# Optimization experiments

Measured on AMD Instinct MI355X. Metric: run time of the kernel, lower is better.

The kernel has to match this reference:

```python
import jax, jax.numpy as jnp
import numpy as np

STRIDE = (1, 1)
PAD = 1


def setup_inputs() -> dict:
    key = jax.random.key(0)
    k1, k2, k3 = jax.random.split(key, 3)
    X = jax.random.normal(k1, (32, 128, 56, 56), dtype=jnp.float32)
    weight = jax.random.normal(k2, (256, 128, 3, 3), dtype=jnp.float32) * 0.05
    bias = jax.random.normal(k3, (256,), dtype=jnp.float32) * 0.05
    return {"X": X, "weight": weight, "bias": bias}


def reference(X, weight, bias):
    # Equivalent to the naive 8-loop conv: standard 2D cross-correlation,
    # NCHW input, OIHW weight, stride 1, padding 1.
    out = jax.lax.conv_general_dilated(
        X, weight,
        window_strides=STRIDE,
        padding=[(PAD, PAD), (PAD, PAD)],
        dimension_numbers=("NCHW", "OIHW", "NCHW"),
    )
    out = out + bias[None, :, None, None]
    return out
```

## Files before the change

kernel.cpp:

```cpp
#include <hip/hip_runtime.h>
#include <hip/hip_bf16.h>


typedef __attribute__((ext_vector_type(8))) _Float16 half8;
typedef __attribute__((ext_vector_type(4))) float floatx4;

#define NN    32
#define CC    128
#define HH    56
#define WW    56
#define KOUT  256
#define HWs   3136
#define HP    58
#define HPP   (HP * HP)
#define XP_SHORTS ((size_t)NN * HPP * CC)
#define WT_SHORTS (36 * 8192)
#define WS_NEED ((XP_SHORTS + WT_SHORTS) * sizeof(short))

__device__ __forceinline__ void gload_lds16(const void* g, void* l) {
    __builtin_amdgcn_global_load_lds(
        (const __attribute__((address_space(1))) unsigned int*)g,
        (__attribute__((address_space(3))) unsigned int*)l, 16, 0, 0);
}

__global__ __launch_bounds__(256) void prep_x2(const float* __restrict__ X,
                                               short* __restrict__ Xp) {
    const int n   = blockIdx.x / HP;
    const int hp  = blockIdx.x % HP;
    const int tid = threadIdx.x;
    short* dst = Xp + ((size_t)n * HPP + (size_t)hp * HP) * CC;

    half8 z = {(_Float16)0.f, (_Float16)0.f, (_Float16)0.f, (_Float16)0.f,
               (_Float16)0.f, (_Float16)0.f, (_Float16)0.f, (_Float16)0.f};

    if (hp == 0 || hp == HP - 1) {
#pragma unroll
        for (int it = 0; it < 4; ++it) {
            const int u = it * 256 + tid;
            if (u < 928) *(half8*)&dst[u * 8] = z;
        }
        return;
    }

    const int h = hp - 1;
    __shared__ float xl[128 * 57];
    const float* src = X + (size_t)n * CC * HWs + h * WW;
#pragma unroll
    for (int i = 0; i < 7; ++i) {
        const int idx = i * 256 + tid;
        const int c   = idx / 14;
        const int w4  = idx - c * 14;
        const floatx4 v = *(const floatx4*)&src[(size_t)c * HWs + w4 * 4];
#pragma unroll
        for (int k = 0; k < 4; ++k) xl[c * 57 + w4 * 4 + k] = v[k];
    }
    __syncthreads();
#pragma unroll
    for (int it = 0; it < 4; ++it) {
        const int u = it * 256 + tid;
        if (u < 896) {
            const int oct = u & 15, w = u >> 4;
            _Float16 v[8];
#pragma unroll
            for (int j = 0; j < 8; ++j)
                v[j] = (_Float16)xl[(oct * 8 + j) * 57 + w];
            *(half8*)&dst[(w + 1) * CC + oct * 8] = *(half8*)v;
        } else if (u < 928) {
            const int q = u - 896;
            const int oct = q & 15;
            const int wpad = (q >> 4) ? (HP - 1) : 0;
            *(half8*)&dst[wpad * CC + oct * 8] = z;
        }
    }
}

__global__ __launch_bounds__(256) void prep_w3(const float* __restrict__ Wsrc,
                                               short* __restrict__ Wt) {
    const int gid = blockIdx.x * 256 + threadIdx.x;
    const int t2  = gid >> 10;
    const int u8  = gid & 1023;
    const int r   = u8 >> 3;
    const int o   = u8 & 7;
    const int rs  = t2 >> 2;
    const int ct  = (t2 >> 1) & 1;
    const int kb  = t2 & 1;
    const int k   = kb * 128 + r;
    const int c0  = ct * 64 + ((o ^ (r & 7)) << 3);
    _Float16 v[8];
#pragma unroll
    for (int j = 0; j < 8; ++j)
        v[j] = (_Float16)Wsrc[((size_t)k * CC + c0 + j) * 9 + rs];
    *(half8*)&Wt[(size_t)t2 * 8192 + u8 * 8] = *(half8*)v;
}

__global__ __launch_bounds__(256, 3) void conv_mfma4(
    const short* __restrict__ Xp, const short* __restrict__ Wt,
    const float* __restrict__ bias, float* __restrict__ out) {

    __shared__ __align__(16) short smem[16384];

    const int tid  = threadIdx.x;
    const int lane = tid & 63;
    const int wid  = tid >> 6;
    const int wr   = wid >> 1;
    const int wc   = wid & 1;
    const int bid  = blockIdx.x;
    const int kblk = blockIdx.y;
    const int pblk = (bid & 7) * 98 + (bid >> 3);

    const int swzoct = (lane & 7) ^ (lane >> 3);
    const short* vsrc[4];
#pragma unroll
    for (int i = 0; i < 4; ++i) {
        const int row = wid * 32 + i * 8 + (lane >> 3);
        const int p   = pblk * 128 + row;
        const int n   = p / HWs;
        const int hw  = p % HWs;
        const int h   = hw / WW;
        const int w   = hw % WW;
        vsrc[i] = Xp + ((size_t)n * HPP + (h + 1) * HP + (w + 1)) * CC + swzoct * 8;
    }

    floatx4 acc[4][4];
#pragma unroll
    for (int i = 0; i < 4; i++)
#pragma unroll
        for (int j = 0; j < 4; j++) acc[i][j] = (floatx4)(0.0f);

    for (int k = 0; k < 18; ++k) {
        const int rs = k >> 1, ct = k & 1;
        const int tap = ((rs / 3 - 1) * HP + (rs % 3 - 1)) * CC + ct * 64;

        if (k) __syncthreads();

        const short* as_ = Wt + (size_t)(k * 2 + kblk) * 8192 + wid * 2048 + lane * 8;
#pragma unroll
        for (int i = 0; i < 4; ++i)
            gload_lds16(as_ + i * 512, &smem[wid * 2048 + i * 512]);
#pragma unroll
        for (int i = 0; i < 4; ++i)
            gload_lds16(vsrc[i] + tap, &smem[8192 + wid * 2048 + i * 512]);

        __syncthreads();

#pragma unroll
        for (int ksub = 0; ksub < 2; ++ksub) {
            const int koct = ksub * 4 + (lane >> 4);
            half8 ah[4], bh[4];
#pragma unroll
            for (int mt = 0; mt < 4; ++mt) {
                const int ar = wr * 64 + mt * 16 + (lane & 15);
                ah[mt] = *(const half8*)&smem[ar * 64 + ((koct ^ (ar & 7)) << 3)];
            }
#pragma unroll
            for (int nt = 0; nt < 4; ++nt) {
                const int br = wc * 64 + nt * 16 + (lane & 15);
                bh[nt] = *(const half8*)&smem[8192 + br * 64 + ((koct ^ (br & 7)) << 3)];
            }
#pragma unroll
            for (int mt = 0; mt < 4; ++mt)
#pragma unroll
                for (int nt = 0; nt < 4; ++nt)
                    acc[mt][nt] = __builtin_amdgcn_mfma_f32_16x16x32_f16(
                        ah[mt], bh[nt], acc[mt][nt], 0, 0, 0);
        }
    }

#pragma unroll
    for (int mt = 0; mt < 4; ++mt) {
        const int ch = kblk * 128 + wr * 64 + mt * 16 + ((lane >> 4) << 2);
#pragma unroll
        for (int nt = 0; nt < 4; ++nt) {
            const int p  = pblk * 128 + wc * 64 + nt * 16 + (lane & 15);
            const int n  = p / HWs;
            const int hw = p % HWs;
            float* ob = out + ((size_t)n * KOUT + ch) * HWs + hw;
#pragma unroll
            for (int r = 0; r < 4; ++r)
                ob[(size_t)r * HWs] = acc[mt][nt][r] + bias[ch + r];
        }
    }
}

__global__ __launch_bounds__(256) void conv_naive(const float* __restrict__ X,
                                                  const float* __restrict__ Wt,
                                                  const float* __restrict__ bias,
                                                  float* __restrict__ out) {
    long o = (long)blockIdx.x * 256 + threadIdx.x;
    int w_ = o % WW;
    long t1 = o / WW;
    int h_ = t1 % HH;
    long t2 = t1 / HH;
    int k_ = t2 % KOUT;
    int n_ = (int)(t2 / KOUT);
    float acc = bias[k_];
    for (int c = 0; c < CC; ++c)
        for (int r = 0; r < 3; ++r) {
            int ih = h_ + r - 1;
            if ((unsigned)ih >= 56u) continue;
            for (int s = 0; s < 3; ++s) {
                int iw = w_ + s - 1;
                if ((unsigned)iw >= 56u) continue;
                acc += X[((long)(n_ * CC + c) * HH + ih) * WW + iw] *
                       Wt[((k_ * CC + c) * 3 + r) * 3 + s];
            }
        }
    out[o] = acc;
}

extern "C" void kernel_launch(void* const* d_in, const int* in_sizes, int n_in,
                              void* d_out, int out_size, void* d_ws, size_t ws_size,
                              hipStream_t stream) {
    const float* X    = (const float*)d_in[0];
    const float* Wsrc = (const float*)d_in[1];
    const float* bias = (const float*)d_in[2];
    float* out        = (float*)d_out;

    if (ws_size >= WS_NEED) {
        short* Xp = (short*)d_ws;
        short* Wt = Xp + XP_SHORTS;
        prep_x2<<<NN * HP, 256, 0, stream>>>(X, Xp);
        prep_w3<<<144, 256, 0, stream>>>(Wsrc, Wt);
        conv_mfma4<<<dim3(784, 2), 256, 0, stream>>>(Xp, Wt, bias, out);
    } else {
        conv_naive<<<100352, 256, 0, stream>>>(X, Wsrc, bias, out);
    }
}
```

Before: 213.3 us.

## Triple-buffer LDS pipeline with 512-thread 256-channel tiles and fused prep kernel

The conv kernel now computes all 256 output channels per block with 8 waves, so the grid no longer splits output channels and each input tile is loaded once. A three-stage LDS ring buffer with split half-loads, vmcnt waits and barriers overlaps global-to-LDS copies with MFMA work. MFMA sections are wrapped in s_setprio. The two prep kernels are merged into one launch, and the weight layout is changed to match. Costs are larger dynamic LDS (144KB), fewer blocks per CU, and a per-call hipFuncSetAttribute on the host.

```diff
diff --git a/kernel.cpp b/kernel.cpp
--- a/kernel.cpp
+++ b/kernel.cpp
@@ -14,8 +14,10 @@
 #define HP    58
 #define HPP   (HP * HP)
 #define XP_SHORTS ((size_t)NN * HPP * CC)
-#define WT_SHORTS (36 * 8192)
+#define WT_SHORTS (18 * 16384)
 #define WS_NEED ((XP_SHORTS + WT_SHORTS) * sizeof(short))
+#define BUF_HALFS 24576
+#define LDS_BYTES (3 * BUF_HALFS * 2)
 
 __device__ __forceinline__ void gload_lds16(const void* g, void* l) {
     __builtin_amdgcn_global_load_lds(
@@ -23,11 +25,33 @@
         (__attribute__((address_space(3))) unsigned int*)l, 16, 0, 0);
 }
 
-__global__ __launch_bounds__(256) void prep_x2(const float* __restrict__ X,
-                                               short* __restrict__ Xp) {
-    const int n   = blockIdx.x / HP;
-    const int hp  = blockIdx.x % HP;
+__global__ __launch_bounds__(256) void prep_fused(const float* __restrict__ X,
+                                                  const float* __restrict__ Wsrc,
+                                                  short* __restrict__ Xp,
+                                                  short* __restrict__ Wt) {
+    __shared__ float xl[128 * 57];
     const int tid = threadIdx.x;
+
+    if (blockIdx.x < 144) {
+        const int gid  = blockIdx.x * 256 + tid;
+        const int tile = gid >> 11;
+        const int u    = gid & 2047;
+        const int r    = u >> 3;
+        const int o    = u & 7;
+        const int tap  = tile >> 1;
+        const int ct   = tile & 1;
+        const int c0   = ct * 64 + ((o ^ (r & 7)) << 3);
+        _Float16 v[8];
+#pragma unroll
+        for (int j = 0; j < 8; ++j)
+            v[j] = (_Float16)Wsrc[((size_t)r * CC + c0 + j) * 9 + tap];
+        *(half8*)&Wt[(size_t)tile * 16384 + u * 8] = *(half8*)v;
+        return;
+    }
+
+    const int xb = blockIdx.x - 144;
+    const int n  = xb / HP;
+    const int hp = xb % HP;
     short* dst = Xp + ((size_t)n * HPP + (size_t)hp * HP) * CC;
 
     half8 z = {(_Float16)0.f, (_Float16)0.f, (_Float16)0.f, (_Float16)0.f,
@@ -43,7 +67,6 @@
     }
 
     const int h = hp - 1;
-    __shared__ float xl[128 * 57];
     const float* src = X + (size_t)n * CC * HWs + h * WW;
 #pragma unroll
     for (int i = 0; i < 7; ++i) {
@@ -74,30 +97,11 @@
     }
 }
 
-__global__ __launch_bounds__(256) void prep_w3(const float* __restrict__ Wsrc,
-                                               short* __restrict__ Wt) {
-    const int gid = blockIdx.x * 256 + threadIdx.x;
-    const int t2  = gid >> 10;
-    const int u8  = gid & 1023;
-    const int r   = u8 >> 3;
-    const int o   = u8 & 7;
-    const int rs  = t2 >> 2;
-    const int ct  = (t2 >> 1) & 1;
-    const int kb  = t2 & 1;
-    const int k   = kb * 128 + r;
-    const int c0  = ct * 64 + ((o ^ (r & 7)) << 3);
-    _Float16 v[8];
-#pragma unroll
-    for (int j = 0; j < 8; ++j)
-        v[j] = (_Float16)Wsrc[((size_t)k * CC + c0 + j) * 9 + rs];
-    *(half8*)&Wt[(size_t)t2 * 8192 + u8 * 8] = *(half8*)v;
-}
-
-__global__ __launch_bounds__(256, 3) void conv_mfma4(
+__global__ __launch_bounds__(512, 2) void conv_mfma5(
     const short* __restrict__ Xp, const short* __restrict__ Wt,
     const float* __restrict__ bias, float* __restrict__ out) {
 
-    __shared__ __align__(16) short smem[16384];
+    extern __shared__ __align__(16) short smem[];
 
     const int tid  = threadIdx.x;
     const int lane = tid & 63;
@@ -105,14 +109,13 @@
     const int wr   = wid >> 1;
     const int wc   = wid & 1;
     const int bid  = blockIdx.x;
-    const int kblk = blockIdx.y;
     const int pblk = (bid & 7) * 98 + (bid >> 3);
 
     const int swzoct = (lane & 7) ^ (lane >> 3);
-    const short* vsrc[4];
-#pragma unroll
-    for (int i = 0; i < 4; ++i) {
-        const int row = wid * 32 + i * 8 + (lane >> 3);
+    const short* vsrc[2];
+#pragma unroll
+    for (int i = 0; i < 2; ++i) {
+        const int row = wid * 16 + i * 8 + (lane >> 3);
         const int p   = pblk * 128 + row;
         const int n   = p / HWs;
         const int hw  = p % HWs;
@@ -121,54 +124,105 @@
         vsrc[i] = Xp + ((size_t)n * HPP + (h + 1) * HP + (w + 1)) * CC + swzoct * 8;
     }
 
+    const int aoff = wid * 2048 + lane * 8;
+
+#define STAGE_P0(kk, bb) do {                                                  \
+    const short* as_ = Wt + (size_t)(kk) * 16384 + aoff;                       \
+    gload_lds16(as_,        &smem[(bb) + aoff]);                               \
+    gload_lds16(as_ + 512,  &smem[(bb) + aoff + 512]);                         \
+    const int rs_ = (kk) >> 1;                                                 \
+    const int tap_ = ((rs_ / 3 - 1) * HP + (rs_ % 3 - 1)) * CC + ((kk) & 1) * 64; \
+    gload_lds16(vsrc[0] + tap_, &smem[(bb) + 16384 + wid * 1024 + lane * 8]);  \
+} while (0)
+#define STAGE_P1(kk, bb) do {                                                  \
+    const short* as_ = Wt + (size_t)(kk) * 16384 + aoff;                       \
+    gload_lds16(as_ + 1024, &smem[(bb) + aoff + 1024]);                        \
+    gload_lds16(as_ + 1536, &smem[(bb) + aoff + 1536]);                        \
+    const int rs_ = (kk) >> 1;                                                 \
+    const int tap_ = ((rs_ / 3 - 1) * HP + (rs_ % 3 - 1)) * CC + ((kk) & 1) * 64; \
+    gload_lds16(vsrc[1] + tap_, &smem[(bb) + 16384 + wid * 1024 + 512 + lane * 8]); \
+} while (0)
+
     floatx4 acc[4][4];
 #pragma unroll
     for (int i = 0; i < 4; i++)
 #pragma unroll
         for (int j = 0; j < 4; j++) acc[i][j] = (floatx4)(0.0f);
 
-    for (int k = 0; k < 18; ++k) {
-        const int rs = k >> 1, ct = k & 1;
-        const int tap = ((rs / 3 - 1) * HP + (rs % 3 - 1)) * CC + ct * 64;
-
-        if (k) __syncthreads();
-
-        const short* as_ = Wt + (size_t)(k * 2 + kblk) * 8192 + wid * 2048 + lane * 8;
-#pragma unroll
-        for (int i = 0; i < 4; ++i)
-            gload_lds16(as_ + i * 512, &smem[wid * 2048 + i * 512]);
-#pragma unroll
-        for (int i = 0; i < 4; ++i)
-            gload_lds16(vsrc[i] + tap, &smem[8192 + wid * 2048 + i * 512]);
-
-        __syncthreads();
-
-#pragma unroll
-        for (int ksub = 0; ksub < 2; ++ksub) {
-            const int koct = ksub * 4 + (lane >> 4);
+    STAGE_P0(0, 0); STAGE_P1(0, 0);
+    STAGE_P0(1, BUF_HALFS); STAGE_P1(1, BUF_HALFS);
+    asm volatile("s_waitcnt vmcnt(6)" ::: "memory");
+    __builtin_amdgcn_sched_barrier(0);
+    __builtin_amdgcn_s_barrier();
+
+    int cur = 0;
+    for (int t = 0; t < 18; ++t) {
+        const int cb  = cur * BUF_HALFS;
+        const int nxt = (cur + 2 >= 3) ? cur - 1 : cur + 2;
+        const int nb  = nxt * BUF_HALFS;
+        const int kk  = (t + 2 < 18) ? t + 2 : 17;
+
+        STAGE_P0(kk, nb);
+        {
+            const int koct = (lane >> 4);
             half8 ah[4], bh[4];
 #pragma unroll
             for (int mt = 0; mt < 4; ++mt) {
                 const int ar = wr * 64 + mt * 16 + (lane & 15);
-                ah[mt] = *(const half8*)&smem[ar * 64 + ((koct ^ (ar & 7)) << 3)];
+                ah[mt] = *(const half8*)&smem[cb + ar * 64 + ((koct ^ (ar & 7)) << 3)];
             }
 #pragma unroll
             for (int nt = 0; nt < 4; ++nt) {
                 const int br = wc * 64 + nt * 16 + (lane & 15);
-                bh[nt] = *(const half8*)&smem[8192 + br * 64 + ((koct ^ (br & 7)) << 3)];
-            }
+                bh[nt] = *(const half8*)&smem[cb + 16384 + br * 64 + ((koct ^ (br & 7)) << 3)];
+            }
+            __builtin_amdgcn_s_setprio(1);
 #pragma unroll
             for (int mt = 0; mt < 4; ++mt)
 #pragma unroll
                 for (int nt = 0; nt < 4; ++nt)
                     acc[mt][nt] = __builtin_amdgcn_mfma_f32_16x16x32_f16(
                         ah[mt], bh[nt], acc[mt][nt], 0, 0, 0);
-        }
-    }
+            __builtin_amdgcn_s_setprio(0);
+        }
+        __builtin_amdgcn_s_barrier();
+
+        STAGE_P1(kk, nb);
+        {
+            const int koct = 4 + (lane >> 4);
+            half8 ah[4], bh[4];
+#pragma unroll
+            for (int mt = 0; mt < 4; ++mt) {
+                const int ar = wr * 64 + mt * 16 + (lane & 15);
+                ah[mt] = *(const half8*)&smem[cb + ar * 64 + ((koct ^ (ar & 7)) << 3)];
+            }
+#pragma unroll
+            for (int nt = 0; nt < 4; ++nt) {
+                const int br = wc * 64 + nt * 16 + (lane & 15);
+                bh[nt] = *(const half8*)&smem[cb + 16384 + br * 64 + ((koct ^ (br & 7)) << 3)];
+            }
+            __builtin_amdgcn_s_setprio(1);
+#pragma unroll
+            for (int mt = 0; mt < 4; ++mt)
+#pragma unroll
+                for (int nt = 0; nt < 4; ++nt)
+                    acc[mt][nt] = __builtin_amdgcn_mfma_f32_16x16x32_f16(
+                        ah[mt], bh[nt], acc[mt][nt], 0, 0, 0);
+            __builtin_amdgcn_s_setprio(0);
+        }
+
+        asm volatile("s_waitcnt vmcnt(6)" ::: "memory");
+        __builtin_amdgcn_sched_barrier(0);
+        __builtin_amdgcn_s_barrier();
+
+        cur = (cur + 1 >= 3) ? 0 : cur + 1;
+    }
+#undef STAGE_P0
+#undef STAGE_P1
 
 #pragma unroll
     for (int mt = 0; mt < 4; ++mt) {
-        const int ch = kblk * 128 + wr * 64 + mt * 16 + ((lane >> 4) << 2);
+        const int ch = wr * 64 + mt * 16 + ((lane >> 4) << 2);
 #pragma unroll
         for (int nt = 0; nt < 4; ++nt) {
             const int p  = pblk * 128 + wc * 64 + nt * 16 + (lane & 15);
@@ -216,12 +270,19 @@
     const float* bias = (const float*)d_in[2];
     float* out        = (float*)d_out;
 
-    if (ws_size >= WS_NEED) {
+    static hipError_t attr_rc = hipFuncSetAttribute(
+        (const void*)conv_mfma5, hipFuncAttributeMaxDynamicSharedMemorySize,
+        LDS_BYTES);
+    hipError_t rc = hipFuncSetAttribute(
+        (const void*)conv_mfma5, hipFuncAttributeMaxDynamicSharedMemorySize,
+        LDS_BYTES);
+    (void)attr_rc;
+
+    if (ws_size >= WS_NEED && rc == hipSuccess) {
         short* Xp = (short*)d_ws;
         short* Wt = Xp + XP_SHORTS;
-        prep_x2<<<NN * HP, 256, 0, stream>>>(X, Xp);
-        prep_w3<<<144, 256, 0, stream>>>(Wsrc, Wt);
-        conv_mfma4<<<dim3(784, 2), 256, 0, stream>>>(Xp, Wt, bias, out);
+        prep_fused<<<144 + NN * HP, 256, 0, stream>>>(X, Wsrc, Xp, Wt);
+        conv_mfma5<<<784, 512, LDS_BYTES, stream>>>(Xp, Wt, bias, out);
     } else {
         conv_naive<<<100352, 256, 0, stream>>>(X, Wsrc, bias, out);
     }
```

Result: no change. 216.5 us (+1.5%).
